# Kernel tuning notes

Hardware: AMD Instinct MI355X
Metric: run time of the kernel (lower is better)

Reference implementation:

```python
import jax, jax.numpy as jnp
import numpy as np

H_BINS = 61
INSZ = 150
EPS = 1e-6


def rgb_uv_hist(img, sigma_u, sigma_v, c):
    """Differentiable RGB-uv soft histogram with per-channel RBF kernels.
    img: [B,3,H,W] in [0,1]; sigma_u, sigma_v, c: [3]. Returns [B,3,h,h]."""
    B = img.shape[0]
    x = jnp.clip(img, 0.0, 1.0).reshape(B, 3, -1)          # [B,3,P]
    Iy = jnp.sqrt(jnp.sum(x * x, axis=1))                  # [B,P] intensity weight
    lg = jnp.log(x + EPS)
    # log-chromaticity (u,v) per reference channel c in {R,G,B}
    u = jnp.stack([lg[:, 0] - lg[:, 1], lg[:, 1] - lg[:, 0], lg[:, 2] - lg[:, 0]], 1)  # [B,3,P]
    v = jnp.stack([lg[:, 0] - lg[:, 2], lg[:, 1] - lg[:, 2], lg[:, 2] - lg[:, 1]], 1)
    bins = jnp.linspace(-3.0, 3.0, H_BINS).astype(img.dtype)
    ku = jnp.exp(-((u[..., None] - bins) ** 2) / (sigma_u[None, :, None, None] ** 2))  # [B,3,P,h]
    kv = jnp.exp(-((v[..., None] - bins) ** 2) / (sigma_v[None, :, None, None] ** 2))
    w = Iy[:, None, :] * c[None, :, None]                  # [B,3,P]
    hist = jnp.einsum('bcpu,bcp,bcpv->bcuv', ku, w, kv)    # [B,3,h,h]
    norm = jnp.sum(hist, axis=(1, 2, 3), keepdims=True) + EPS
    return hist / norm


def _conv(x, w, b, stride):
    y = jax.lax.conv_general_dilated(x, w, (stride, stride), 'VALID',
                                     dimension_numbers=('NCHW', 'OIHW', 'NCHW'))
    return jax.nn.relu(y + b[None, :, None, None])


def _head(hist, w1, b1, w2, b2, w3, b3, fc):
    z = _conv(hist, w1, b1, 2)   # 61 -> 29
    z = _conv(z, w2, b2, 2)      # 29 -> 14
    z = _conv(z, w3, b3, 1)      # 14 -> 13
    z = z.reshape(z.shape[0], -1)  # [B, 512*13*13]
    return jnp.abs(z @ fc.T)


def setup_inputs() -> dict:
    key = jax.random.key(0)
    ks = jax.random.split(key, 16)
    B = 16
    d = {}
    d['image'] = jax.random.uniform(ks[0], (B, 3, INSZ, INSZ), jnp.float32)
    # hist params: sigmas in a numerically reasonable range (orig init: random()*0.02)
    d['su_s'] = 0.05 + 0.2 * jax.random.uniform(ks[1], (3,), jnp.float32)
    d['sv_s'] = 0.05 + 0.2 * jax.random.uniform(ks[2], (3,), jnp.float32)
    d['c_s'] = jnp.ones((3,), jnp.float32)
    d['w1_s'] = 0.05 * jax.random.normal(ks[3], (128, 3, 5, 5), jnp.float32)
    d['b1_s'] = jnp.zeros((128,), jnp.float32)
    d['w2_s'] = 0.02 * jax.random.normal(ks[4], (256, 128, 3, 3), jnp.float32)
    d['b2_s'] = jnp.zeros((256,), jnp.float32)
    d['w3_s'] = 0.02 * jax.random.normal(ks[5], (512, 256, 2, 2), jnp.float32)
    d['b3_s'] = jnp.zeros((512,), jnp.float32)
    d['fc_s'] = 0.003 * jax.random.normal(ks[6], (9, 512 * 13 * 13), jnp.float32)
    d['su_i'] = 0.05 + 0.2 * jax.random.uniform(ks[7], (3,), jnp.float32)
    d['sv_i'] = 0.05 + 0.2 * jax.random.uniform(ks[8], (3,), jnp.float32)
    d['c_i'] = jnp.ones((3,), jnp.float32)
    d['w1_i'] = 0.05 * jax.random.normal(ks[9], (128, 3, 5, 5), jnp.float32)
    d['b1_i'] = jnp.zeros((128,), jnp.float32)
    d['w2_i'] = 0.02 * jax.random.normal(ks[10], (256, 128, 3, 3), jnp.float32)
    d['b2_i'] = jnp.zeros((256,), jnp.float32)
    d['w3_i'] = 0.02 * jax.random.normal(ks[11], (512, 256, 2, 2), jnp.float32)
    d['b3_i'] = jnp.zeros((512,), jnp.float32)
    d['fc_i'] = 0.003 * jax.random.normal(ks[12], (3, 512 * 13 * 13), jnp.float32)
    return d


def reference(image, su_s, sv_s, c_s, w1_s, b1_s, w2_s, b2_s, w3_s, b3_s, fc_s,
              su_i, sv_i, c_i, w1_i, b1_i, w2_i, b2_i, w3_i, b3_i, fc_i):
    B = image.shape[0]
    # sensor branch: hist -> CNN -> |fc| -> 3x3 matrix (transposed), L1-row-norm scaled
    hs = rgb_uv_hist(image, su_s, sv_s, c_s)
    m = _head(hs, w1_s, b1_s, w2_s, b2_s, w3_s, b3_s, fc_s).reshape(B, 3, 3)
    m = jnp.swapaxes(m, -1, -2)                               # .t()
    n = jnp.max(jnp.sum(jnp.abs(m), axis=-1), axis=-1) + 1e-4  # max L1 row norm, [B]
    m = m / n[:, None, None]
    # color mapping: pixels @ m^T
    mapped = jnp.einsum('bjhw,bij->bihw', image, m)
    # illuminant branch on mapped image
    hi = rgb_uv_hist(mapped, su_i, sv_i, c_i)
    ill = _head(hi, w1_i, b1_i, w2_i, b2_i, w3_i, b3_i, fc_i)  # [B,3]
    est_ill = jnp.einsum('bij,bj->bi', jnp.linalg.inv(m), ill)
    return est_ill
```

## Files before the change

kernel.cpp:

```cpp
#include <hip/hip_runtime.h>

#define P_PIX 22500
#define HB 61
#define HSP 28
#define PPB 832
#define NCHK 7

typedef float f32x4 __attribute__((ext_vector_type(4)));
typedef _Float16 f16x8 __attribute__((ext_vector_type(8)));
typedef _Float16 f16x4 __attribute__((ext_vector_type(4)));

__global__ __launch_bounds__(256) void hist_mfma(
    const float* __restrict__ img, const float* __restrict__ su,
    const float* __restrict__ sv, const float* __restrict__ cw,
    const float* __restrict__ msc, float* __restrict__ hpart)
{
    const int bc = blockIdx.x;
    const int b = bc / 3, c = bc % 3;
    const int split = blockIdx.y;
    const int tid  = threadIdx.x;
    const int wv   = tid >> 6;
    const int lane = tid & 63;
    const int quad = lane >> 4;
    const int mr   = lane & 15;

    __shared__ __align__(16) _Float16 B_lds[8192];
    __shared__ float suu[128], svv[128], sww[128];

    const float sig_u = su[c], sig_v = sv[c];
    const float inv_su2 = 1.f / (sig_u * sig_u);
    const float inv_sv2 = 1.f / (sig_v * sig_v);
    const float cwc = cw[c];
    const float ubin_b = -3.f + 0.1f * (float)lane;
    const float ubin_a = -3.f + 0.1f * (float)(wv * 16 + mr);

    const bool hasM = (msc != nullptr);
    float m00=0,m01=0,m02=0,m10=0,m11=0,m12=0,m20=0,m21=0,m22=0;
    if (hasM) {
        const float* mp = msc + b * 9;
        m00=mp[0]; m01=mp[1]; m02=mp[2];
        m10=mp[3]; m11=mp[4]; m12=mp[5];
        m20=mp[6]; m21=mp[7]; m22=mp[8];
    }

    const int p0   = split * PPB;
    const int pend = min(p0 + PPB, P_PIX);

    f32x4 acc[4];
#pragma unroll
    for (int nt = 0; nt < 4; ++nt) acc[nt] = (f32x4){0.f, 0.f, 0.f, 0.f};

    for (int chunk = 0; chunk < NCHK; ++chunk) {
        __syncthreads();
        if (tid < 128) {
            int px = p0 + chunk * 128 + tid;
            float u = 0.f, v = 0.f, wgt = 0.f;
            if (px < pend) {
                const float* ip = img + (size_t)b * 3 * P_PIX + px;
                float r = ip[0], g = ip[P_PIX], bl = ip[2 * P_PIX];
                if (hasM) {
                    float r2 = m00 * r + m01 * g + m02 * bl;
                    float g2 = m10 * r + m11 * g + m12 * bl;
                    float b2 = m20 * r + m21 * g + m22 * bl;
                    r = r2; g = g2; bl = b2;
                }
                r  = fminf(fmaxf(r, 0.f), 1.f);
                g  = fminf(fmaxf(g, 0.f), 1.f);
                bl = fminf(fmaxf(bl, 0.f), 1.f);
                float Iy = sqrtf(r * r + g * g + bl * bl);
                float lr = __logf(r + 1e-6f);
                float lg = __logf(g + 1e-6f);
                float lb = __logf(bl + 1e-6f);
                if (c == 0)      { u = lr - lg; v = lr - lb; }
                else if (c == 1) { u = lg - lr; v = lg - lb; }
                else             { u = lb - lr; v = lb - lg; }
                wgt = Iy * cwc;
            }
            suu[tid] = u; svv[tid] = v; sww[tid] = wgt;
        }
        __syncthreads();
#pragma unroll
        for (int r = 0; r < 4; ++r) {
            int pg = wv + 4 * r;
            f32x4 v0 = *(const f32x4*)&svv[pg * 8];
            f32x4 v1 = *(const f32x4*)&svv[pg * 8 + 4];
            f16x8 bv;
#pragma unroll
            for (int j = 0; j < 4; ++j) {
                float dv = v0[j] - ubin_b;
                bv[j] = (_Float16)__expf(-dv * dv * inv_sv2);
                float dv1 = v1[j] - ubin_b;
                bv[4 + j] = (_Float16)__expf(-dv1 * dv1 * inv_sv2);
            }
            *(f16x8*)&B_lds[(pg * 64 + lane) * 8] = bv;
        }
        f16x8 af[4];
#pragma unroll
        for (int kk = 0; kk < 4; ++kk) {
            int pxg = kk * 4 + quad;
            f32x4 u0 = *(const f32x4*)&suu[pxg * 8];
            f32x4 u1 = *(const f32x4*)&suu[pxg * 8 + 4];
            f32x4 w0 = *(const f32x4*)&sww[pxg * 8];
            f32x4 w1 = *(const f32x4*)&sww[pxg * 8 + 4];
#pragma unroll
            for (int j = 0; j < 4; ++j) {
                float du = u0[j] - ubin_a;
                af[kk][j] = (_Float16)(__expf(-du * du * inv_su2) * w0[j]);
                float du1 = u1[j] - ubin_a;
                af[kk][4 + j] = (_Float16)(__expf(-du1 * du1 * inv_su2) * w1[j]);
            }
        }
        __syncthreads();
#pragma unroll
        for (int kk = 0; kk < 4; ++kk) {
            int pgq = kk * 4 + quad;
#pragma unroll
            for (int nt = 0; nt < 4; ++nt) {
                f16x8 bvv = *(const f16x8*)&B_lds[(pgq * 64 + nt * 16 + mr) * 8];
                acc[nt] = __builtin_amdgcn_mfma_f32_16x16x32_f16(af[kk], bvv, acc[nt], 0, 0, 0);
            }
        }
    }

    float* hp = hpart + ((size_t)bc * HSP + split) * 4096;
#pragma unroll
    for (int nt = 0; nt < 4; ++nt) {
        int v = nt * 16 + mr;
#pragma unroll
        for (int r = 0; r < 4; ++r) {
            int u = wv * 16 + quad * 4 + r;
            hp[u * 64 + v] = acc[nt][r];
        }
    }
}

__global__ __launch_bounds__(256) void reduce_hist(
    const float* __restrict__ hpart, float* __restrict__ hist,
    float* __restrict__ hsum3)
{
    const int bc = blockIdx.x;
    const int part = blockIdx.y;
    const int tid = threadIdx.x;
    const float* base = hpart + (size_t)bc * HSP * 4096;
    float lsum = 0.f;
#pragma unroll
    for (int t = 0; t < 4; ++t) {
        int idx = part * 1024 + t * 256 + tid;
        int u = idx >> 6, v = idx & 63;
        float s = 0.f;
        for (int sp = 0; sp < HSP; ++sp) s += base[sp * 4096 + idx];
        if (u < HB && v < HB) {
            hist[(size_t)bc * (HB * HB) + u * HB + v] = s;
            lsum += s;
        }
    }
    __shared__ float red[4];
    for (int off = 32; off; off >>= 1) lsum += __shfl_down(lsum, off, 64);
    if ((tid & 63) == 0) red[tid >> 6] = lsum;
    __syncthreads();
    if (tid == 0) atomicAdd(&hsum3[bc], red[0] + red[1] + red[2] + red[3]);
}

__global__ __launch_bounds__(256) void conv1_mfma(
    const float* __restrict__ hist, const float* __restrict__ hsum3,
    const _Float16* __restrict__ w1h, const float* __restrict__ bias,
    _Float16* __restrict__ out)
{
    const int b    = blockIdx.x;
    const int m0   = blockIdx.y * 128;
    const int tid  = threadIdx.x;
    const int wv   = tid >> 6;
    const int lane = tid & 63;
    const int quad = lane >> 4;
    const int mr   = lane & 15;

    __shared__ __align__(16) _Float16 A_lds[128 * 96];

    const float sc = 1.f / (hsum3[b * 3] + hsum3[b * 3 + 1] + hsum3[b * 3 + 2] + 1e-6f);
    const float* inb = hist + (size_t)b * 3 * 3721;

    for (int slot = tid; slot < 1536; slot += 256) {
        int m  = slot & 127;
        int kg = slot >> 7;
        int mg = m0 + m;
        bool mok = (mg < 841);
        int oh = mok ? mg / 29 : 0;
        int ow = mok ? mg % 29 : 0;
        const float* pbase = inb + (oh * 2) * 61 + (ow * 2);
        f16x8 av;
#pragma unroll
        for (int j = 0; j < 8; ++j) {
            int k = kg * 8 + j;
            float x = 0.f;
            if (mok && k < 75) {
                int ci = k / 25, r = k % 25;
                int kh = r / 5, kw = r % 5;
                x = pbase[ci * 3721 + kh * 61 + kw] * sc;
            }
            av[j] = (_Float16)x;
        }
        *(f16x8*)&A_lds[(kg * 128 + m) * 8] = av;
    }
    __syncthreads();

    f16x8 wf[3][2];
#pragma unroll
    for (int ks = 0; ks < 3; ++ks)
#pragma unroll
        for (int nt = 0; nt < 2; ++nt) {
            int co = (wv * 2 + nt) * 16 + mr;
            wf[ks][nt] = *(const f16x8*)&w1h[co * 96 + ks * 32 + quad * 8];
        }

    f32x4 acc[8][2];
#pragma unroll
    for (int mt = 0; mt < 8; ++mt)
#pragma unroll
        for (int nt = 0; nt < 2; ++nt) acc[mt][nt] = (f32x4){0.f, 0.f, 0.f, 0.f};

#pragma unroll
    for (int ks = 0; ks < 3; ++ks)
#pragma unroll
        for (int mt = 0; mt < 8; ++mt) {
            f16x8 bv = *(const f16x8*)&A_lds[((ks * 4 + quad) * 128 + mt * 16 + mr) * 8];
#pragma unroll
            for (int nt = 0; nt < 2; ++nt)
                acc[mt][nt] = __builtin_amdgcn_mfma_f32_16x16x32_f16(bv, wf[ks][nt], acc[mt][nt], 0, 0, 0);
        }

#pragma unroll
    for (int mt = 0; mt < 8; ++mt) {
#pragma unroll
        for (int r = 0; r < 4; ++r) {
            int sp = m0 + mt * 16 + quad * 4 + r;
            if (sp >= 841) continue;
#pragma unroll
            for (int nt = 0; nt < 2; ++nt) {
                int co = (wv * 2 + nt) * 16 + mr;
                float y = acc[mt][nt][r] + bias[co];
                out[((size_t)b * 841 + sp) * 128 + co] = (_Float16)fmaxf(y, 0.f);
            }
        }
    }
}

template<int CIN, int COUT, int Kk, int S, int IN, int OUT,
         int NPB, int KSPL, int KCH>
__global__ __launch_bounds__(256) void conv_mfma(
    const _Float16* __restrict__ in_h,
    const _Float16* __restrict__ w_h,
    float* __restrict__ out)
{
    constexpr int KK   = Kk * Kk;
    constexpr int OSZ  = OUT * OUT;
    constexpr int MT   = (OSZ + 15) / 16;
    constexpr int MP   = MT * 16;
    constexpr int KTOT = CIN * KK;
    constexpr int KC   = KTOT / KSPL;
    constexpr int NCHUNK = KC / KCH;
    constexpr int NT   = NPB / 64;
    constexpr int KSN  = KCH / 32;
    constexpr int SLOTS = MP * (KCH / 8);

    const int b   = blockIdx.x;
    const int co0 = blockIdx.y * NPB;
    const int k00 = blockIdx.z * KC;
    const int tid  = threadIdx.x;
    const int wv   = tid >> 6;
    const int lane = tid & 63;
    const int quad = lane >> 4;
    const int mr   = lane & 15;

    __shared__ __align__(16) _Float16 A_lds[MP * KCH];

    const _Float16* inb = in_h + (size_t)b * (IN * IN) * CIN;
    float* outp = out + (size_t)blockIdx.z * gridDim.x * OSZ * COUT;

    f32x4 acc[MT][NT];
#pragma unroll
    for (int mt = 0; mt < MT; ++mt)
#pragma unroll
        for (int nt = 0; nt < NT; ++nt) acc[mt][nt] = (f32x4){0.f, 0.f, 0.f, 0.f};

    for (int ch = 0; ch < NCHUNK; ++ch) {
        const int k0 = k00 + ch * KCH;
        __syncthreads();
        for (int slot = tid; slot < SLOTS; slot += 256) {
            int m  = slot % MP;
            int kg = slot / MP;
            bool mok = (m < OSZ);
            int oh = mok ? m / OUT : 0;
            int ow = mok ? m % OUT : 0;
            int kbase = k0 + kg * 8;
            int khkw = kbase / CIN;
            int ci0  = kbase % CIN;
            int kh = khkw / Kk, kw = khkw % Kk;
            f16x8 av = (f16x8)(_Float16)0.f;
            if (mok)
                av = *(const f16x8*)&inb[((size_t)((oh * S + kh) * IN + (ow * S + kw))) * CIN + ci0];
            *(f16x8*)&A_lds[(kg * MP + m) * 8] = av;
        }
        __syncthreads();
        f16x8 wf[KSN][NT];
#pragma unroll
        for (int ks = 0; ks < KSN; ++ks)
#pragma unroll
            for (int nt = 0; nt < NT; ++nt) {
                int co = co0 + (wv * NT + nt) * 16 + mr;
                wf[ks][nt] = *(const f16x8*)&w_h[(size_t)co * KTOT + k0 + ks * 32 + quad * 8];
            }
#pragma unroll
        for (int ks = 0; ks < KSN; ++ks) {
#pragma unroll
            for (int mt = 0; mt < MT; ++mt) {
                f16x8 bv = *(const f16x8*)&A_lds[((ks * 4 + quad) * MP + mt * 16 + mr) * 8];
#pragma unroll
                for (int nt = 0; nt < NT; ++nt)
                    acc[mt][nt] = __builtin_amdgcn_mfma_f32_16x16x32_f16(bv, wf[ks][nt], acc[mt][nt], 0, 0, 0);
            }
        }
    }

#pragma unroll
    for (int mt = 0; mt < MT; ++mt) {
#pragma unroll
        for (int r = 0; r < 4; ++r) {
            int sp = mt * 16 + quad * 4 + r;
            if (sp >= OSZ) continue;
#pragma unroll
            for (int nt = 0; nt < NT; ++nt) {
                int co = co0 + (wv * NT + nt) * 16 + mr;
                outp[((size_t)b * OSZ + sp) * COUT + co] = acc[mt][nt][r];
            }
        }
    }
}

__global__ __launch_bounds__(256) void reduce_bias_relu_f16(
    const float* __restrict__ p, const float* __restrict__ bias,
    _Float16* __restrict__ out, int cout, int total4, int kspl, int total)
{
    for (int i4 = blockIdx.x * 256 + threadIdx.x; i4 < total4; i4 += gridDim.x * 256) {
        f32x4 s = (f32x4){0.f, 0.f, 0.f, 0.f};
        for (int ks = 0; ks < kspl; ++ks)
            s += *(const f32x4*)&p[(size_t)ks * total + i4 * 4];
        f32x4 bb = *(const f32x4*)&bias[(i4 * 4) % cout];
        f16x4 o;
#pragma unroll
        for (int j = 0; j < 4; ++j) o[j] = (_Float16)fmaxf(s[j] + bb[j], 0.f);
        *(f16x4*)&out[(size_t)i4 * 4] = o;
    }
}

__global__ __launch_bounds__(256) void reduce_bias_relu(
    const float* __restrict__ p, const float* __restrict__ bias,
    float* __restrict__ out, int cout, int total4, int kspl, int total)
{
    for (int i4 = blockIdx.x * 256 + threadIdx.x; i4 < total4; i4 += gridDim.x * 256) {
        f32x4 s = (f32x4){0.f, 0.f, 0.f, 0.f};
        for (int ks = 0; ks < kspl; ++ks)
            s += *(const f32x4*)&p[(size_t)ks * total + i4 * 4];
        f32x4 bb = *(const f32x4*)&bias[(i4 * 4) % cout];
        f32x4 o;
#pragma unroll
        for (int j = 0; j < 4; ++j) o[j] = fmaxf(s[j] + bb[j], 0.f);
        *(f32x4*)&out[(size_t)i4 * 4] = o;
    }
}

__global__ __launch_bounds__(256) void prep_weights(
    const float* __restrict__ w1s, const float* __restrict__ w1i,
    const float* __restrict__ w2s, const float* __restrict__ w3s,
    const float* __restrict__ w2i, const float* __restrict__ w3i,
    const float* __restrict__ fcs, const float* __restrict__ fci,
    _Float16* __restrict__ w1h, _Float16* __restrict__ w23,
    float* __restrict__ fct)
{
    const int R1 = 24576;
    const int N2 = 294912, N3 = 524288;
    const int R2 = 2 * (N2 + N3);
    const int K = 86528;
    const int R3 = 12 * K;
    const int T = R1 + R2 + R3;
    for (int i = blockIdx.x * 256 + threadIdx.x; i < T; i += gridDim.x * 256) {
        if (i < R1) {
            int br = i / 12288, r = i % 12288;
            int co = r / 96, k = r % 96;
            const float* s = br ? w1i : w1s;
            w1h[i] = (k < 75) ? (_Float16)s[co * 75 + k] : (_Float16)0.f;
        } else if (i < R1 + R2) {
            int j = i - R1;
            int out_idx = j;
            const float* s; int CK, KKn;
            if (j < N2)                { s = w2s; CK = 1152; KKn = 9; }
            else if (j < N2 + N3)      { s = w3s; j -= N2; CK = 1024; KKn = 4; }
            else if (j < 2 * N2 + N3)  { s = w2i; j -= N2 + N3; CK = 1152; KKn = 9; }
            else                       { s = w3i; j -= 2 * N2 + N3; CK = 1024; KKn = 4; }
            int co = j / CK, rem = j % CK;
            int ci = rem % (CK / KKn), khkw = rem / (CK / KKn);
            w23[out_idx] = (_Float16)s[co * CK + ci * KKn + khkw];
        } else {
            int j = i - R1 - R2;
            int o = j / K, rem = j % K;
            int sp = rem / 512, co = rem % 512;
            const float* s = (o < 9) ? (fcs + o * K) : (fci + (o - 9) * K);
            fct[j] = s[co * 169 + sp];
        }
    }
}

__global__ __launch_bounds__(256) void fc_atomic(
    const float* __restrict__ z, const float* __restrict__ fcw,
    float* __restrict__ out, int Kdim, int NO, int KSPL)
{
    const int b = blockIdx.x, o = blockIdx.y, ks = blockIdx.z;
    const int kchunk = Kdim / KSPL;
    const int k0 = ks * kchunk;
    const f32x4* zp = (const f32x4*)(z + (size_t)b * Kdim + k0);
    const f32x4* wp = (const f32x4*)(fcw + (size_t)o * Kdim + k0);
    const int n4 = kchunk / 4;
    f32x4 s4 = (f32x4){0.f, 0.f, 0.f, 0.f};
    for (int k = threadIdx.x; k < n4; k += 256) {
        f32x4 a = zp[k], w = wp[k];
        s4 += a * w;
    }
    float s = s4[0] + s4[1] + s4[2] + s4[3];
    __shared__ float red[4];
    for (int off = 32; off; off >>= 1) s += __shfl_down(s, off, 64);
    if ((threadIdx.x & 63) == 0) red[threadIdx.x >> 6] = s;
    __syncthreads();
    if (threadIdx.x == 0)
        atomicAdd(&out[(size_t)b * NO + o], red[0] + red[1] + red[2] + red[3]);
}

__global__ void build_m(const float* __restrict__ h, float* __restrict__ msc)
{
    int b = threadIdx.x;
    if (b < 16) {
        float m[9];
#pragma unroll
        for (int i = 0; i < 3; ++i)
#pragma unroll
            for (int j = 0; j < 3; ++j) m[i * 3 + j] = fabsf(h[b * 9 + j * 3 + i]);
        float n = 0.f;
#pragma unroll
        for (int i = 0; i < 3; ++i) {
            float r = m[i * 3] + m[i * 3 + 1] + m[i * 3 + 2];
            n = fmaxf(n, r);
        }
        n += 1e-4f;
        float inv = 1.f / n;
#pragma unroll
        for (int k = 0; k < 9; ++k) msc[b * 9 + k] = m[k] * inv;
    }
}

__global__ void final_est(const float* __restrict__ msc, const float* __restrict__ ill,
                          float* __restrict__ out)
{
    int bidx = threadIdx.x;
    if (bidx < 16) {
        const float* m = msc + bidx * 9;
        float a = m[0], b = m[1], c = m[2];
        float d = m[3], e = m[4], f = m[5];
        float g = m[6], h = m[7], i = m[8];
        float A = e * i - f * h, B = f * g - d * i, C = d * h - e * g;
        float D = c * h - b * i, E = a * i - c * g, F = b * g - a * h;
        float G = b * f - c * e, H = c * d - a * f, I = a * e - b * d;
        float det = a * A + b * B + c * C;
        float inv_det = 1.f / det;
        float x0 = fabsf(ill[bidx * 3 + 0]);
        float x1 = fabsf(ill[bidx * 3 + 1]);
        float x2 = fabsf(ill[bidx * 3 + 2]);
        out[bidx * 3 + 0] = (A * x0 + D * x1 + G * x2) * inv_det;
        out[bidx * 3 + 1] = (B * x0 + E * x1 + H * x2) * inv_det;
        out[bidx * 3 + 2] = (C * x0 + F * x1 + I * x2) * inv_det;
    }
}

extern "C" void kernel_launch(void* const* d_in, const int* in_sizes, int n_in,
                              void* d_out, int out_size, void* d_ws, size_t ws_size,
                              hipStream_t stream)
{
    (void)in_sizes; (void)n_in; (void)out_size; (void)ws_size;
    const float* image = (const float*)d_in[0];
    const float* su_s  = (const float*)d_in[1];
    const float* sv_s  = (const float*)d_in[2];
    const float* c_s   = (const float*)d_in[3];
    const float* w1_s  = (const float*)d_in[4];
    const float* b1_s  = (const float*)d_in[5];
    const float* w2_s  = (const float*)d_in[6];
    const float* b2_s  = (const float*)d_in[7];
    const float* w3_s  = (const float*)d_in[8];
    const float* b3_s  = (const float*)d_in[9];
    const float* fc_s  = (const float*)d_in[10];
    const float* su_i  = (const float*)d_in[11];
    const float* sv_i  = (const float*)d_in[12];
    const float* c_i   = (const float*)d_in[13];
    const float* w1_i  = (const float*)d_in[14];
    const float* b1_i  = (const float*)d_in[15];
    const float* w2_i  = (const float*)d_in[16];
    const float* b2_i  = (const float*)d_in[17];
    const float* w3_i  = (const float*)d_in[18];
    const float* b3_i  = (const float*)d_in[19];
    const float* fc_i  = (const float*)d_in[20];

    float* W     = (float*)d_ws;
    float* hist  = W;
    float* o3    = hist + 178608;
    float* hd    = o3 + 1384448;
    float* hsum3 = hd + 144;
    float* msc   = hsum3 + 48;
    float* fct   = msc + 144;
    float* p2    = fct + 1038336;
    float* p3    = p2 + 3211264;
    float* hpart = p3 + 2768896;
    _Float16* o1h   = (_Float16*)(hpart + 48 * HSP * 4096);
    _Float16* o2h   = o1h   + 1722368;
    _Float16* w2h_s = o2h   + 802816;
    _Float16* w3h_s = w2h_s + 294912;
    _Float16* w2h_i = w3h_s + 524288;
    _Float16* w3h_i = w2h_i + 294912;
    _Float16* w1h_s = w3h_i + 524288;
    _Float16* w1h_i = w1h_s + 12288;

    const int FCK = 512 * 13 * 13;
    const int O2_TOT = 16 * 196 * 256;
    const int O3_TOT = 16 * 169 * 512;
    float* fct_s = fct;
    float* fct_i = fct + 9 * FCK;

    prep_weights<<<1024, 256, 0, stream>>>(w1_s, w1_i, w2_s, w3_s, w2_i, w3_i,
                                           fc_s, fc_i, w1h_s, w2h_s, fct);

    hipMemsetAsync(hd, 0, 192 * 4, stream);
    hist_mfma<<<dim3(48, HSP), 256, 0, stream>>>(image, su_s, sv_s, c_s, nullptr, hpart);
    reduce_hist<<<dim3(48, 4), 256, 0, stream>>>(hpart, hist, hsum3);
    conv1_mfma<<<dim3(16, 7), 256, 0, stream>>>(hist, hsum3, w1h_s, b1_s, o1h);
    conv_mfma<128, 256, 3, 2, 29, 14, 128, 4, 96><<<dim3(16, 2, 4), 256, 0, stream>>>(o1h, w2h_s, p2);
    reduce_bias_relu_f16<<<784, 256, 0, stream>>>(p2, b2_s, o2h, 256, O2_TOT / 4, 4, O2_TOT);
    conv_mfma<256, 512, 2, 1, 14, 13, 128, 2, 64><<<dim3(16, 4, 2), 256, 0, stream>>>(o2h, w3h_s, p3);
    reduce_bias_relu<<<1024, 256, 0, stream>>>(p3, b3_s, o3, 512, O3_TOT / 4, 2, O3_TOT);
    fc_atomic<<<dim3(16, 9, 8), 256, 0, stream>>>(o3, fct_s, hd, FCK, 9, 8);
    build_m<<<1, 64, 0, stream>>>(hd, msc);

    hipMemsetAsync(hd, 0, 192 * 4, stream);
    hist_mfma<<<dim3(48, HSP), 256, 0, stream>>>(image, su_i, sv_i, c_i, msc, hpart);
    reduce_hist<<<dim3(48, 4), 256, 0, stream>>>(hpart, hist, hsum3);
    conv1_mfma<<<dim3(16, 7), 256, 0, stream>>>(hist, hsum3, w1h_i, b1_i, o1h);
    conv_mfma<128, 256, 3, 2, 29, 14, 128, 4, 96><<<dim3(16, 2, 4), 256, 0, stream>>>(o1h, w2h_i, p2);
    reduce_bias_relu_f16<<<784, 256, 0, stream>>>(p2, b2_i, o2h, 256, O2_TOT / 4, 4, O2_TOT);
    conv_mfma<256, 512, 2, 1, 14, 13, 128, 2, 64><<<dim3(16, 4, 2), 256, 0, stream>>>(o2h, w3h_i, p3);
    reduce_bias_relu<<<1024, 256, 0, stream>>>(p3, b3_i, o3, 512, O3_TOT / 4, 2, O3_TOT);
    fc_atomic<<<dim3(16, 3, 8), 256, 0, stream>>>(o3, fct_i, hd, FCK, 3, 8);
    final_est<<<1, 64, 0, stream>>>(msc, hd, (float*)d_out);
}
```

Measured before the change: 376.1 us.

## Run final FC layers on fp16 MFMA and retune histogram split

The fp32 FC dot-product kernel is replaced with an MFMA kernel that reads fp16 activations and fp16 pre-transposed FC weights. It works on 16 batches by 16 outputs by 512 K per block, reduces in LDS and finishes with atomics. The conv3 epilogue now writes fp16 output, which halves the memory traffic for activations and weights. The histogram kernel's split is also retuned to fewer splits with more pixels per block. The cost is reduced FC precision, since fp16 inputs feed into the 3x3 matrix inversion.

Result: faster. 358.7 us (-4.6%).

```diff
diff --git a/kernel.cpp b/kernel.cpp
--- a/kernel.cpp
+++ b/kernel.cpp
@@ -2,9 +2,9 @@
 
 #define P_PIX 22500
 #define HB 61
-#define HSP 28
-#define PPB 832
-#define NCHK 7
+#define HSP 21
+#define PPB 1152
+#define NCHK 9
 
 typedef float f32x4 __attribute__((ext_vector_type(4)));
 typedef _Float16 f16x8 __attribute__((ext_vector_type(8)));
@@ -352,19 +352,38 @@
     }
 }
 
-__global__ __launch_bounds__(256) void reduce_bias_relu(
-    const float* __restrict__ p, const float* __restrict__ bias,
-    float* __restrict__ out, int cout, int total4, int kspl, int total)
-{
-    for (int i4 = blockIdx.x * 256 + threadIdx.x; i4 < total4; i4 += gridDim.x * 256) {
-        f32x4 s = (f32x4){0.f, 0.f, 0.f, 0.f};
-        for (int ks = 0; ks < kspl; ++ks)
-            s += *(const f32x4*)&p[(size_t)ks * total + i4 * 4];
-        f32x4 bb = *(const f32x4*)&bias[(i4 * 4) % cout];
-        f32x4 o;
-#pragma unroll
-        for (int j = 0; j < 4; ++j) o[j] = fmaxf(s[j] + bb[j], 0.f);
-        *(f32x4*)&out[(size_t)i4 * 4] = o;
+__global__ __launch_bounds__(256) void fc_mfma(
+    const _Float16* __restrict__ z,
+    const _Float16* __restrict__ fcw,
+    float* __restrict__ out, int NO)
+{
+    const int tid  = threadIdx.x;
+    const int wv   = tid >> 6;
+    const int lane = tid & 63;
+    const int quad = lane >> 4;
+    const int mr   = lane & 15;
+    const int kw0  = blockIdx.x * 512 + wv * 128;
+
+    __shared__ float sred[1024];
+
+    f32x4 acc = (f32x4){0.f, 0.f, 0.f, 0.f};
+    const bool bok = (mr < NO);
+#pragma unroll
+    for (int ks = 0; ks < 4; ++ks) {
+        int kk = kw0 + ks * 32 + quad * 8;
+        f16x8 av = *(const f16x8*)&z[(size_t)mr * 86528 + kk];
+        f16x8 bw = (f16x8)(_Float16)0.f;
+        if (bok) bw = *(const f16x8*)&fcw[(size_t)mr * 86528 + kk];
+        acc = __builtin_amdgcn_mfma_f32_16x16x32_f16(av, bw, acc, 0, 0, 0);
+    }
+#pragma unroll
+    for (int r = 0; r < 4; ++r)
+        sred[wv * 256 + (quad * 4 + r) * 16 + mr] = acc[r];
+    __syncthreads();
+    if (tid < 256) {
+        float s = sred[tid] + sred[256 + tid] + sred[512 + tid] + sred[768 + tid];
+        int o = tid & 15, b = tid >> 4;
+        if (o < NO) atomicAdd(&out[b * NO + o], s);
     }
 }
 
@@ -374,7 +393,7 @@
     const float* __restrict__ w2i, const float* __restrict__ w3i,
     const float* __restrict__ fcs, const float* __restrict__ fci,
     _Float16* __restrict__ w1h, _Float16* __restrict__ w23,
-    float* __restrict__ fct)
+    _Float16* __restrict__ fch)
 {
     const int R1 = 24576;
     const int N2 = 294912, N3 = 524288;
@@ -404,33 +423,9 @@
             int o = j / K, rem = j % K;
             int sp = rem / 512, co = rem % 512;
             const float* s = (o < 9) ? (fcs + o * K) : (fci + (o - 9) * K);
-            fct[j] = s[co * 169 + sp];
-        }
-    }
-}
-
-__global__ __launch_bounds__(256) void fc_atomic(
-    const float* __restrict__ z, const float* __restrict__ fcw,
-    float* __restrict__ out, int Kdim, int NO, int KSPL)
-{
-    const int b = blockIdx.x, o = blockIdx.y, ks = blockIdx.z;
-    const int kchunk = Kdim / KSPL;
-    const int k0 = ks * kchunk;
-    const f32x4* zp = (const f32x4*)(z + (size_t)b * Kdim + k0);
-    const f32x4* wp = (const f32x4*)(fcw + (size_t)o * Kdim + k0);
-    const int n4 = kchunk / 4;
-    f32x4 s4 = (f32x4){0.f, 0.f, 0.f, 0.f};
-    for (int k = threadIdx.x; k < n4; k += 256) {
-        f32x4 a = zp[k], w = wp[k];
-        s4 += a * w;
-    }
-    float s = s4[0] + s4[1] + s4[2] + s4[3];
-    __shared__ float red[4];
-    for (int off = 32; off; off >>= 1) s += __shfl_down(s, off, 64);
-    if ((threadIdx.x & 63) == 0) red[threadIdx.x >> 6] = s;
-    __syncthreads();
-    if (threadIdx.x == 0)
-        atomicAdd(&out[(size_t)b * NO + o], red[0] + red[1] + red[2] + red[3]);
+            fch[j] = (_Float16)s[co * 169 + sp];
+        }
+    }
 }
 
 __global__ void build_m(const float* __restrict__ h, float* __restrict__ msc)
@@ -507,31 +502,29 @@
 
     float* W     = (float*)d_ws;
     float* hist  = W;
-    float* o3    = hist + 178608;
-    float* hd    = o3 + 1384448;
+    float* hd    = hist + 178608;
     float* hsum3 = hd + 144;
     float* msc   = hsum3 + 48;
-    float* fct   = msc + 144;
-    float* p2    = fct + 1038336;
+    float* p2    = msc + 144;
     float* p3    = p2 + 3211264;
     float* hpart = p3 + 2768896;
     _Float16* o1h   = (_Float16*)(hpart + 48 * HSP * 4096);
     _Float16* o2h   = o1h   + 1722368;
-    _Float16* w2h_s = o2h   + 802816;
+    _Float16* o3h   = o2h   + 802816;
+    _Float16* fch   = o3h   + 1384448;
+    _Float16* w2h_s = fch   + 1038336;
     _Float16* w3h_s = w2h_s + 294912;
     _Float16* w2h_i = w3h_s + 524288;
     _Float16* w3h_i = w2h_i + 294912;
     _Float16* w1h_s = w3h_i + 524288;
     _Float16* w1h_i = w1h_s + 12288;
 
-    const int FCK = 512 * 13 * 13;
     const int O2_TOT = 16 * 196 * 256;
     const int O3_TOT = 16 * 169 * 512;
-    float* fct_s = fct;
-    float* fct_i = fct + 9 * FCK;
+    const int FCK = 86528;
 
     prep_weights<<<1024, 256, 0, stream>>>(w1_s, w1_i, w2_s, w3_s, w2_i, w3_i,
-                                           fc_s, fc_i, w1h_s, w2h_s, fct);
+                                           fc_s, fc_i, w1h_s, w2h_s, fch);
 
     hipMemsetAsync(hd, 0, 192 * 4, stream);
     hist_mfma<<<dim3(48, HSP), 256, 0, stream>>>(image, su_s, sv_s, c_s, nullptr, hpart);
@@ -540,8 +533,8 @@
     conv_mfma<128, 256, 3, 2, 29, 14, 128, 4, 96><<<dim3(16, 2, 4), 256, 0, stream>>>(o1h, w2h_s, p2);
     reduce_bias_relu_f16<<<784, 256, 0, stream>>>(p2, b2_s, o2h, 256, O2_TOT / 4, 4, O2_TOT);
     conv_mfma<256, 512, 2, 1, 14, 13, 128, 2, 64><<<dim3(16, 4, 2), 256, 0, stream>>>(o2h, w3h_s, p3);
-    reduce_bias_relu<<<1024, 256, 0, stream>>>(p3, b3_s, o3, 512, O3_TOT / 4, 2, O3_TOT);
-    fc_atomic<<<dim3(16, 9, 8), 256, 0, stream>>>(o3, fct_s, hd, FCK, 9, 8);
+    reduce_bias_relu_f16<<<1024, 256, 0, stream>>>(p3, b3_s, o3h, 512, O3_TOT / 4, 2, O3_TOT);
+    fc_mfma<<<169, 256, 0, stream>>>(o3h, fch, hd, 9);
     build_m<<<1, 64, 0, stream>>>(hd, msc);
 
     hipMemsetAsync(hd, 0, 192 * 4, stream);
@@ -551,7 +544,7 @@
     conv_mfma<128, 256, 3, 2, 29, 14, 128, 4, 96><<<dim3(16, 2, 4), 256, 0, stream>>>(o1h, w2h_i, p2);
     reduce_bias_relu_f16<<<784, 256, 0, stream>>>(p2, b2_i, o2h, 256, O2_TOT / 4, 4, O2_TOT);
     conv_mfma<256, 512, 2, 1, 14, 13, 128, 2, 64><<<dim3(16, 4, 2), 256, 0, stream>>>(o2h, w3h_i, p3);
-    reduce_bias_relu<<<1024, 256, 0, stream>>>(p3, b3_i, o3, 512, O3_TOT / 4, 2, O3_TOT);
-    fc_atomic<<<dim3(16, 3, 8), 256, 0, stream>>>(o3, fct_i, hd, FCK, 3, 8);
+    reduce_bias_relu_f16<<<1024, 256, 0, stream>>>(p3, b3_i, o3h, 512, O3_TOT / 4, 2, O3_TOT);
+    fc_mfma<<<169, 256, 0, stream>>>(o3h, fch + 9 * FCK, hd, 3);
     final_est<<<1, 64, 0, stream>>>(msc, hd, (float*)d_out);
 }
```
